# Optimization experiments

Hardware: AMD Instinct MI355X
Metric: run time of the kernel (lower is better)

## Reference

```python
import jax, jax.numpy as jnp
import numpy as np

N, D, E, OUT = 10000, 15, 320, 30
H_INOUT = 5  # n_heads for in/out attention layers


def mha(q, k, v, wqkv, bqkv, wo, bo, nheads):
    # q,k,v: [B, L, E]; torch.nn.MultiheadAttention math (unbatched per node)
    B, L, Ed = q.shape
    hd = Ed // nheads
    wq, wk, wv = jnp.split(wqkv, 3, axis=0)
    bq, bk, bv = jnp.split(bqkv, 3)
    q2 = (q @ wq.T + bq).reshape(B, L, nheads, hd)
    k2 = (k @ wk.T + bk).reshape(B, -1, nheads, hd)
    v2 = (v @ wv.T + bv).reshape(B, -1, nheads, hd)
    scores = jnp.einsum('blhd,bmhd->bhlm', q2, k2) * (hd ** -0.5)
    a = jax.nn.softmax(scores, axis=-1)
    o = jnp.einsum('bhlm,bmhd->blhd', a, v2).reshape(B, L, Ed)
    return o @ wo.T + bo


def attn_layer(seq, Wq, Wk, Wv, wqkv, bqkv, wo, bo, nheads):
    # AttentionLayer: custom Q/K/V projections then MultiheadAttention
    return mha(seq @ Wq, seq @ Wk, seq @ Wv, wqkv, bqkv, wo, bo, nheads)


def setup_inputs() -> dict:
    key = jax.random.key(0)
    ks = jax.random.split(key, 24)
    s = 0.05  # scale params small for numerically stable softmax
    inp = {
        'X': jax.random.normal(ks[0], (N, E), jnp.float32),
        'in_idx': jax.random.randint(ks[1], (N, D), 0, N),
        'out_idx': jax.random.randint(ks[2], (N, D), 0, N),
        'in_Wq': jax.random.uniform(ks[3], (E, E)) * s,
        'in_Wk': jax.random.uniform(ks[4], (E, E)) * s,
        'in_Wv': jax.random.uniform(ks[5], (E, E)) * s,
        'in_qkv_w': jax.random.normal(ks[6], (3 * E, E)) * s,
        'in_qkv_b': jax.random.normal(ks[7], (3 * E,)) * s,
        'in_o_w': jax.random.normal(ks[8], (E, E)) * s,
        'in_o_b': jax.random.normal(ks[9], (E,)) * s,
        'out_Wq': jax.random.uniform(ks[10], (E, E)) * s,
        'out_Wk': jax.random.uniform(ks[11], (E, E)) * s,
        'out_Wv': jax.random.uniform(ks[12], (E, E)) * s,
        'out_qkv_w': jax.random.normal(ks[13], (3 * E, E)) * s,
        'out_qkv_b': jax.random.normal(ks[14], (3 * E,)) * s,
        'out_o_w': jax.random.normal(ks[15], (E, E)) * s,
        'out_o_b': jax.random.normal(ks[16], (E,)) * s,
        'fin_qkv_w': jax.random.normal(ks[17], (3 * E, E)) * s,
        'fin_qkv_b': jax.random.normal(ks[18], (3 * E,)) * s,
        'fin_o_w': jax.random.normal(ks[19], (E, E)) * s,
        'fin_o_b': jax.random.normal(ks[20], (E,)) * s,
        'W': jax.random.uniform(ks[21], (E, OUT)) * s,
    }
    return inp


def reference(X, in_idx, out_idx, in_Wq, in_Wk, in_Wv, in_qkv_w, in_qkv_b,
              in_o_w, in_o_b, out_Wq, out_Wk, out_Wv, out_qkv_w, out_qkv_b,
              out_o_w, out_o_b, fin_qkv_w, fin_qkv_b, fin_o_w, fin_o_b, W):
    # per-node sequence: [self ; neighbors] -> [N, D+1, E]
    seq_in = jnp.concatenate([X[:, None, :], X[in_idx]], axis=1)
    seq_out = jnp.concatenate([X[:, None, :], X[out_idx]], axis=1)
    a_in = attn_layer(seq_in, in_Wq, in_Wk, in_Wv, in_qkv_w, in_qkv_b,
                      in_o_w, in_o_b, H_INOUT)
    a_out = attn_layer(seq_out, out_Wq, out_Wk, out_Wv, out_qkv_w, out_qkv_b,
                       out_o_w, out_o_b, H_INOUT)
    att = jnp.concatenate([a_in, a_out], axis=1)  # [N, 2(D+1), E]
    fin = mha(att, att, att, fin_qkv_w, fin_qkv_b, fin_o_w, fin_o_b, 1)
    # first token of final attention per node -> project -> ELU
    return jax.nn.elu(fin[:, 0, :] @ W)
```

## Files before the change

### kernel.cpp

```cpp
#include <hip/hip_runtime.h>
#include <hip/hip_bf16.h>

typedef __hip_bfloat16 bf16;
typedef __bf16 nbf;
typedef nbf bf16x8 __attribute__((ext_vector_type(8)));
typedef float f32x4 __attribute__((ext_vector_type(4)));

#define NNODE 10000
#define DDEG  15
#define EE    320
#define LL    16
#define NH    5
#define HD    64
#define OUTD  30
#define PCOLS 1920
#define KF    642
#define TSTB  648

__global__ void detect_dtype_kernel(const unsigned int* __restrict__ X, int* __restrict__ flag)
{
    __shared__ int cnt;
    if (threadIdx.x == 0) cnt = 0;
    __syncthreads();
    int local = 0;
    for (int i = threadIdx.x; i < 1024; i += 256) {
        unsigned int lo = X[i] & 0xFFFFu;
        int e = (int)((lo >> 7) & 0xFFu);
        if (e >= 100 && e <= 140) local++;
    }
    atomicAdd(&cnt, local);
    __syncthreads();
    if (threadIdx.x == 0) *flag = (cnt > 512) ? 1 : 0;
}

__global__ void convert_bf_kernel(const void* __restrict__ src, nbf* __restrict__ dst,
                                  int n, const int* __restrict__ flag)
{
    int i = blockIdx.x * 256 + threadIdx.x;
    if (i >= n) return;
    if (*flag) dst[i] = ((const nbf*)src)[i];
    else       dst[i] = (nbf)(((const float*)src)[i]);
}

#define NSEG 18
struct ConvTab {
    const void* src[NSEG];
    void*       dst[NSEG];
    int         n[NSEG];
    int         tobf[NSEG];
};

__global__ void convert_batch_kernel(ConvTab t, const int* __restrict__ flag)
{
    const int seg = blockIdx.y;
    const int i = blockIdx.x * 256 + threadIdx.x;
    if (i >= t.n[seg]) return;
    float v = (*flag) ? (float)(((const nbf*)t.src[seg])[i]) : ((const float*)t.src[seg])[i];
    if (t.tobf[seg]) ((nbf*)t.dst[seg])[i] = (nbf)v;
    else             ((float*)t.dst[seg])[i] = v;
}

__global__ __launch_bounds__(256) void transpose3_kernel(const void* s0, const void* s1,
        const void* s2, nbf* __restrict__ dstbase, const int* __restrict__ flag)
{
    const void* src = (blockIdx.z == 0) ? s0 : (blockIdx.z == 1) ? s1 : s2;
    nbf* dst = dstbase + (size_t)blockIdx.z * EE * EE;
    __shared__ nbf tile[32][33];
    const int bx = blockIdx.x * 32, by = blockIdx.y * 32;
    const int tx = threadIdx.x & 31, ty = threadIdx.x >> 5;
    const int f = *flag;
    #pragma unroll
    for (int i = 0; i < 4; ++i) {
        const int r = by + ty + i * 8;
        float v = f ? (float)(((const nbf*)src)[(long)r * EE + bx + tx])
                    : ((const float*)src)[(long)r * EE + bx + tx];
        tile[ty + i * 8][tx] = (nbf)v;
    }
    __syncthreads();
    #pragma unroll
    for (int i = 0; i < 4; ++i) {
        const int r = bx + ty + i * 8;
        dst[(long)r * EE + by + tx] = tile[tx][ty + i * 8];
    }
}

__device__ __forceinline__ void stor(float* p, float v) { *p = v; }
__device__ __forceinline__ void stor(bf16* p, float v) { *p = __float2bfloat16(v); }

template<bool AT, bool BT, typename OT>
__global__ __launch_bounds__(256) void gemm_k(const float* __restrict__ A, int lda,
                       const float* __restrict__ B, int ldb,
                       const float* __restrict__ bias,
                       OT* __restrict__ C, int ldc, int M, int Nn, int K)
{
    __shared__ float As[16][65];
    __shared__ float Bs[16][65];
    const int tid = threadIdx.x;
    const int tx = tid & 15, ty = tid >> 4;
    const int n0 = blockIdx.x * 64, m0 = blockIdx.y * 64;
    float acc[4][4] = {};
    for (int k0 = 0; k0 < K; k0 += 16) {
        if constexpr (AT) {
            for (int i = tid; i < 1024; i += 256) {
                int kk = i >> 6, r = i & 63;
                int gm = m0 + r, gk = k0 + kk;
                As[kk][r] = (gm < M && gk < K) ? A[(long)gk * lda + gm] : 0.f;
            }
        } else {
            for (int i = tid; i < 1024; i += 256) {
                int r = i >> 4, kk = i & 15;
                int gm = m0 + r, gk = k0 + kk;
                As[kk][r] = (gm < M && gk < K) ? A[(long)gm * lda + gk] : 0.f;
            }
        }
        if constexpr (BT) {
            for (int i = tid; i < 1024; i += 256) {
                int r = i >> 4, kk = i & 15;
                int gn = n0 + r, gk = k0 + kk;
                Bs[kk][r] = (gn < Nn && gk < K) ? B[(long)gn * ldb + gk] : 0.f;
            }
        } else {
            for (int i = tid; i < 1024; i += 256) {
                int kk = i >> 6, c = i & 63;
                int gk = k0 + kk, gn = n0 + c;
                Bs[kk][c] = (gk < K && gn < Nn) ? B[(long)gk * ldb + gn] : 0.f;
            }
        }
        __syncthreads();
        #pragma unroll
        for (int kk = 0; kk < 16; ++kk) {
            float ra[4], rb[4];
            #pragma unroll
            for (int a = 0; a < 4; ++a) ra[a] = As[kk][ty * 4 + a];
            #pragma unroll
            for (int b = 0; b < 4; ++b) rb[b] = Bs[kk][tx * 4 + b];
            #pragma unroll
            for (int a = 0; a < 4; ++a)
                #pragma unroll
                for (int b = 0; b < 4; ++b)
                    acc[a][b] += ra[a] * rb[b];
        }
        __syncthreads();
    }
    #pragma unroll
    for (int a = 0; a < 4; ++a) {
        int gm = m0 + ty * 4 + a;
        if (gm >= M) continue;
        #pragma unroll
        for (int b = 0; b < 4; ++b) {
            int gn = n0 + tx * 4 + b;
            if (gn >= Nn) continue;
            float v = acc[a][b] + (bias ? bias[gn] : 0.f);
            stor(&C[(long)gm * ldc + gn], v);
        }
    }
}

template<typename OT>
__global__ __launch_bounds__(256) void gemm_mfma(const nbf* __restrict__ A, int lda,
        const nbf* __restrict__ Bt, int ldb, const float* __restrict__ bias,
        OT* __restrict__ C, int ldc, int M, int Nn, int K)
{
    __shared__ __align__(16) nbf As[128][40];
    __shared__ __align__(16) nbf Bs[128][40];
    const int tid = threadIdx.x;
    const int lane = tid & 63, wave = tid >> 6;
    const int wr = (wave >> 1) * 64, wc = (wave & 1) * 64;
    const int m0 = blockIdx.y * 128, n0 = blockIdx.x * 128;
    const int lr = lane & 15, lq = lane >> 4;
    f32x4 acc[4][4];
    #pragma unroll
    for (int i = 0; i < 4; ++i)
        #pragma unroll
        for (int j = 0; j < 4; ++j) { acc[i][j][0]=0.f; acc[i][j][1]=0.f; acc[i][j][2]=0.f; acc[i][j][3]=0.f; }

    for (int k0 = 0; k0 < K; k0 += 32) {
        #pragma unroll
        for (int v = tid; v < 512; v += 256) {
            const int row = v >> 2, cv = (v & 3) << 3;
            const int gk = k0 + cv;
            {
                const int gm = m0 + row;
                bf16x8 val;
                if (gm < M && gk + 8 <= K) {
                    val = *(const bf16x8*)(A + (long)gm * lda + gk);
                } else {
                    union { bf16x8 v8; nbf e[8]; } u;
                    #pragma unroll
                    for (int j = 0; j < 8; ++j) {
                        float x = (gm < M && gk + j < K) ? (float)A[(long)gm * lda + gk + j] : 0.f;
                        u.e[j] = (nbf)x;
                    }
                    val = u.v8;
                }
                *(bf16x8*)&As[row][cv] = val;
            }
            {
                const int gn = n0 + row;
                bf16x8 val;
                if (gn < Nn && gk + 8 <= K) {
                    val = *(const bf16x8*)(Bt + (long)gn * ldb + gk);
                } else {
                    union { bf16x8 v8; nbf e[8]; } u;
                    #pragma unroll
                    for (int j = 0; j < 8; ++j) {
                        float x = (gn < Nn && gk + j < K) ? (float)Bt[(long)gn * ldb + gk + j] : 0.f;
                        u.e[j] = (nbf)x;
                    }
                    val = u.v8;
                }
                *(bf16x8*)&Bs[row][cv] = val;
            }
        }
        __syncthreads();
        bf16x8 af[4], bfv[4];
        #pragma unroll
        for (int i = 0; i < 4; ++i) af[i] = *(const bf16x8*)&As[wr + i * 16 + lr][lq * 8];
        #pragma unroll
        for (int j = 0; j < 4; ++j) bfv[j] = *(const bf16x8*)&Bs[wc + j * 16 + lr][lq * 8];
        #pragma unroll
        for (int i = 0; i < 4; ++i)
            #pragma unroll
            for (int j = 0; j < 4; ++j)
                acc[i][j] = __builtin_amdgcn_mfma_f32_16x16x32_bf16(af[i], bfv[j], acc[i][j], 0, 0, 0);
        __syncthreads();
    }
    #pragma unroll
    for (int i = 0; i < 4; ++i) {
        #pragma unroll
        for (int j = 0; j < 4; ++j) {
            const int gn = n0 + wc + j * 16 + lr;
            if (gn >= Nn) continue;
            const float bv = bias ? bias[gn] : 0.f;
            #pragma unroll
            for (int r = 0; r < 4; ++r) {
                const int gm = m0 + wr + i * 16 + lq * 4 + r;
                if (gm < M) stor(&C[(long)gm * ldc + gn], acc[i][j][r] + bv);
            }
        }
    }
}

#define NJOB 11
struct JobTab {
    const nbf* A[NJOB];
    const nbf* B[NJOB];
    nbf*       C[NJOB];
};

__global__ __launch_bounds__(256) void gemm_mfma_jobs(JobTab jt)
{
    const nbf* A  = jt.A[blockIdx.z];
    const nbf* Bt = jt.B[blockIdx.z];
    nbf* C        = jt.C[blockIdx.z];
    __shared__ __align__(16) nbf As[128][40];
    __shared__ __align__(16) nbf Bs[128][40];
    const int tid = threadIdx.x;
    const int lane = tid & 63, wave = tid >> 6;
    const int wr = (wave >> 1) * 64, wc = (wave & 1) * 64;
    const int m0 = blockIdx.y * 128, n0 = blockIdx.x * 128;
    const int lr = lane & 15, lq = lane >> 4;
    f32x4 acc[4][4];
    #pragma unroll
    for (int i = 0; i < 4; ++i)
        #pragma unroll
        for (int j = 0; j < 4; ++j) { acc[i][j][0]=0.f; acc[i][j][1]=0.f; acc[i][j][2]=0.f; acc[i][j][3]=0.f; }
    for (int k0 = 0; k0 < EE; k0 += 32) {
        #pragma unroll
        for (int v = tid; v < 512; v += 256) {
            const int row = v >> 2, cv = (v & 3) << 3;
            const int gk = k0 + cv;
            const int gm = m0 + row, gn = n0 + row;
            bf16x8 va = {}, vb = {};
            if (gm < EE) va = *(const bf16x8*)(A + (long)gm * EE + gk);
            if (gn < EE) vb = *(const bf16x8*)(Bt + (long)gn * EE + gk);
            *(bf16x8*)&As[row][cv] = va;
            *(bf16x8*)&Bs[row][cv] = vb;
        }
        __syncthreads();
        bf16x8 af[4], bfv[4];
        #pragma unroll
        for (int i = 0; i < 4; ++i) af[i] = *(const bf16x8*)&As[wr + i * 16 + lr][lq * 8];
        #pragma unroll
        for (int j = 0; j < 4; ++j) bfv[j] = *(const bf16x8*)&Bs[wc + j * 16 + lr][lq * 8];
        #pragma unroll
        for (int i = 0; i < 4; ++i)
            #pragma unroll
            for (int j = 0; j < 4; ++j)
                acc[i][j] = __builtin_amdgcn_mfma_f32_16x16x32_bf16(af[i], bfv[j], acc[i][j], 0, 0, 0);
        __syncthreads();
    }
    #pragma unroll
    for (int i = 0; i < 4; ++i)
        #pragma unroll
        for (int j = 0; j < 4; ++j) {
            const int gn = n0 + wc + j * 16 + lr;
            if (gn >= EE) continue;
            #pragma unroll
            for (int r = 0; r < 4; ++r) {
                const int gm = m0 + wr + i * 16 + lq * 4 + r;
                if (gm < EE) C[(long)gm * EE + gn] = (nbf)acc[i][j][r];
            }
        }
}

__global__ __launch_bounds__(320) void compose_bias_kernel(
        const float* __restrict__ in_o_b, const float* __restrict__ out_o_b,
        const float* __restrict__ fin_qkv_w, const float* __restrict__ fin_qkv_b,
        float* __restrict__ bqc_in, nbf* __restrict__ Kcat, nbf* __restrict__ VcatN)
{
    const int which = blockIdx.x;
    const int b = threadIdx.x;
    const float* ob = (which == 2 || which == 4) ? out_o_b : in_o_b;
    const int off = (which == 0) ? 0 : (which <= 2) ? 320 : 640;
    float acc = fin_qkv_b[off + b];
    const float* wr = fin_qkv_w + (long)(off + b) * EE;
    for (int e = 0; e < EE; ++e) acc += ob[e] * wr[e];
    if (which == 0)      bqc_in[b] = acc;
    else if (which == 1) Kcat[(long)640 * EE + b] = (nbf)acc;
    else if (which == 2) Kcat[(long)641 * EE + b] = (nbf)acc;
    else if (which == 3) VcatN[(long)640 * EE + b] = (nbf)acc;
    else                 VcatN[(long)641 * EE + b] = (nbf)acc;
}

__global__ void compose_bfin(const float* __restrict__ fin_o_b, const float* __restrict__ W,
                             float* __restrict__ bfin)
{
    int j = threadIdx.x;
    if (j >= OUTD) return;
    float acc = 0.f;
    for (int e = 0; e < EE; ++e) acc += fin_o_b[e] * W[e * OUTD + j];
    bfin[j] = acc;
}

__global__ void compose_bT(const float* __restrict__ bqc, const nbf* __restrict__ Kcat,
                           float* __restrict__ bT)
{
    int c = blockIdx.x * 256 + threadIdx.x;
    if (c >= KF) return;
    const nbf* kr = Kcat + (long)c * EE;
    float acc = 0.f;
    for (int b = 0; b < EE; ++b) acc += bqc[b] * (float)kr[b];
    bT[c] = acc;
}

__global__ void ut_prep_kernel(const float* __restrict__ WWT, nbf* __restrict__ Ut)
{
    int v = blockIdx.x * 256 + threadIdx.x;
    if (v >= 64 * EE) return;
    int n = v / EE, e = v % EE;
    float val = 0.f;
    if (n < OUTD) val = WWT[(long)n * KF + e];
    else if (n >= 32 && n < 32 + OUTD) val = WWT[(long)(n - 32) * KF + 320 + e];
    Ut[v] = (nbf)val;
}

__global__ __launch_bounds__(256) void row0_kernel(const nbf* __restrict__ P,
        const int* __restrict__ in_idx, nbf* __restrict__ Orow0)
{
    const int tid = threadIdx.x, lane = tid & 63, wave = tid >> 6;
    const int node = blockIdx.x * 4 + wave;
    __shared__ float a_sh[4][16];
    __shared__ int srcs_sh[4][16];
    const int m = lane & 15, q4 = lane >> 4;
    const int src = (m == 0) ? node : in_idx[node * DDEG + m - 1];
    if (q4 == 0) srcs_sh[wave][m] = src;
    const nbf* qrow = P + (long)node * PCOLS;
    const nbf* krow = P + (long)src * PCOLS + 320;
    #pragma unroll
    for (int h = 0; h < NH; ++h) {
        float s = 0.f;
        bf16x8 q1 = *(const bf16x8*)(qrow + h * 64 + q4 * 16);
        bf16x8 q2 = *(const bf16x8*)(qrow + h * 64 + q4 * 16 + 8);
        bf16x8 k1 = *(const bf16x8*)(krow + h * 64 + q4 * 16);
        bf16x8 k2 = *(const bf16x8*)(krow + h * 64 + q4 * 16 + 8);
        #pragma unroll
        for (int j = 0; j < 8; ++j)
            s += (float)q1[j] * (float)k1[j] + (float)q2[j] * (float)k2[j];
        s += __shfl_xor(s, 16);
        s += __shfl_xor(s, 32);
        s *= 0.125f;
        float mxv = s;
        #pragma unroll
        for (int msk = 8; msk >= 1; msk >>= 1) mxv = fmaxf(mxv, __shfl_xor(mxv, msk));
        float e = __expf(s - mxv);
        float es = e;
        #pragma unroll
        for (int msk = 8; msk >= 1; msk >>= 1) es += __shfl_xor(es, msk);
        if (q4 == 0) a_sh[wave][m] = e / es;
        float o = 0.f;
        #pragma unroll
        for (int mm = 0; mm < 16; ++mm)
            o += a_sh[wave][mm] * (float)P[(long)srcs_sh[wave][mm] * PCOLS + 640 + h * 64 + lane];
        Orow0[(long)node * EE + h * 64 + lane] = (nbf)o;
    }
}

__global__ __launch_bounds__(320) void attn_y_kernel(const nbf* __restrict__ P,
        const int* __restrict__ in_idx, const int* __restrict__ out_idx,
        const nbf* __restrict__ Tb, const nbf* __restrict__ Ut,
        float* __restrict__ Ygl, int node_base)
{
    const int bx = blockIdx.x;
    const int lnode = bx >> 1, d = bx & 1;
    const int node = node_base + lnode;
    const int tid = threadIdx.x;
    const int lane = tid & 63, wave = tid >> 6;
    __shared__ __align__(16) nbf v_s[16][328];
    __shared__ __align__(16) nbf p_s[NH][16][16];
    __shared__ float Yp[NH][16][32];
    const int* idx = d ? out_idx : in_idx;
    const long coloff = (long)d * 960;
    const int lr = lane & 15, lq = lane >> 4;
    #pragma unroll
    for (int v = tid; v < 640; v += 320) {
        const int row = v / 40, c8 = (v % 40) * 8;
        const int src = (row == 0) ? node : idx[node * DDEG + row - 1];
        *(bf16x8*)&v_s[row][c8] = *(const bf16x8*)(P + (long)src * PCOLS + coloff + 640 + c8);
    }
    const int msrc = (lr == 0) ? node : idx[node * DDEG + lr - 1];
    const nbf* prow = P + (long)msrc * PCOLS + coloff;
    f32x4 sc = {0.f, 0.f, 0.f, 0.f};
    #pragma unroll
    for (int c = 0; c < 2; ++c) {
        bf16x8 aq = *(const bf16x8*)(prow + wave * 64 + c * 32 + lq * 8);
        bf16x8 bk = *(const bf16x8*)(prow + 320 + wave * 64 + c * 32 + lq * 8);
        sc = __builtin_amdgcn_mfma_f32_16x16x32_bf16(aq, bk, sc, 0, 0, 0);
    }
    float pr[4], mx4[4], sm4[4];
    #pragma unroll
    for (int r = 0; r < 4; ++r) { pr[r] = sc[r] * 0.125f; mx4[r] = pr[r]; }
    #pragma unroll
    for (int msk = 8; msk >= 1; msk >>= 1)
        #pragma unroll
        for (int r = 0; r < 4; ++r) mx4[r] = fmaxf(mx4[r], __shfl_xor(mx4[r], msk));
    #pragma unroll
    for (int r = 0; r < 4; ++r) { pr[r] = __expf(pr[r] - mx4[r]); sm4[r] = pr[r]; }
    #pragma unroll
    for (int msk = 8; msk >= 1; msk >>= 1)
        #pragma unroll
        for (int r = 0; r < 4; ++r) sm4[r] += __shfl_xor(sm4[r], msk);
    #pragma unroll
    for (int r = 0; r < 4; ++r) p_s[wave][lq * 4 + r][lr] = (nbf)(pr[r] / sm4[r]);
    union { bf16x8 v8; nbf e[8]; } pf;
    #pragma unroll
    for (int j = 0; j < 8; ++j) pf.e[j] = (nbf)0.f;
    if (lq < 2) pf.v8 = *(const bf16x8*)&p_s[wave][lr][lq * 8];
    __syncthreads();
    #pragma unroll
    for (int t = 0; t < 4; ++t) {
        const int e0 = wave * 64 + t * 16;
        union { bf16x8 v8; nbf e[8]; } af;
        #pragma unroll
        for (int j = 0; j < 8; ++j) af.e[j] = (nbf)0.f;
        if (lq < 2) {
            #pragma unroll
            for (int j = 0; j < 8; ++j) af.e[j] = v_s[lq * 8 + j][e0 + lr];
        }
        f32x4 ov = {0.f, 0.f, 0.f, 0.f};
        ov = __builtin_amdgcn_mfma_f32_16x16x32_bf16(af.v8, pf.v8, ov, 0, 0, 0);
        union { unsigned long long u; nbf e[4]; } o4;
        #pragma unroll
        for (int r = 0; r < 4; ++r) o4.e[r] = (nbf)ov[r];
        *(unsigned long long*)&v_s[lr][e0 + lq * 4] = o4.u;
    }
    const nbf* Utd = Ut + (long)d * 32 * EE;
    const nbf* TbRow = Tb + (long)node * TSTB + (long)d * 320;
    f32x4 yacc[2];
    yacc[0][0]=0.f; yacc[0][1]=0.f; yacc[0][2]=0.f; yacc[0][3]=0.f;
    yacc[1][0]=0.f; yacc[1][1]=0.f; yacc[1][2]=0.f; yacc[1][3]=0.f;
    const int e0w = wave * 64;
    #pragma unroll
    for (int c = 0; c < 2; ++c) {
        const int kk = e0w + c * 32 + lq * 8;
        bf16x8 afy = *(const bf16x8*)&v_s[lr][kk];
        #pragma unroll
        for (int nt = 0; nt < 2; ++nt) {
            const int row = nt * 16 + lr;
            const nbf* bp = (row == 31) ? (TbRow + kk) : (Utd + (long)row * EE + kk);
            bf16x8 bfy = *(const bf16x8*)bp;
            yacc[nt] = __builtin_amdgcn_mfma_f32_16x16x32_bf16(afy, bfy, yacc[nt], 0, 0, 0);
        }
    }
    #pragma unroll
    for (int nt = 0; nt < 2; ++nt)
        #pragma unroll
        for (int r = 0; r < 4; ++r)
            Yp[wave][lq * 4 + r][nt * 16 + lr] = yacc[nt][r];
    __syncthreads();
    float* yout = Ygl + (long)(lnode * 2 + d) * 512;
    for (int v = tid; v < 512; v += 320) {
        float sme = 0.f;
        #pragma unroll
        for (int w = 0; w < NH; ++w) sme += Yp[w][v >> 5][v & 31];
        yout[v] = sme;
    }
}

__global__ __launch_bounds__(256) void combine_kernel(const float* __restrict__ Ygl,
        const nbf* __restrict__ Tb, const float* __restrict__ WWT,
        const float* __restrict__ bfin, void* __restrict__ out,
        long obase, int cnt, const int* __restrict__ flag)
{
    const int tid = threadIdx.x, lane = tid & 63, wave = tid >> 6;
    const int node = blockIdx.x * 4 + wave;
    const int nodec = (node < cnt) ? node : (cnt - 1);
    __shared__ float Yl[4][1024];
    __shared__ float sf[4][32];
    const float* ysrc = Ygl + (long)nodec * 1024;
    #pragma unroll
    for (int v = lane; v < 1024; v += 64) Yl[wave][v] = ysrc[v];
    if (lane < 32) {
        const int d = lane >> 4, m = lane & 15;
        sf[wave][lane] = (Yl[wave][d * 512 + m * 32 + 31]
                          + (float)Tb[(long)nodec * TSTB + 640 + d]) * 0.05590169943749474f;
    }
    float mx = -1e30f;
    #pragma unroll 4
    for (int m = 0; m < 32; ++m) mx = fmaxf(mx, sf[wave][m]);
    float esum = 0.f, a_in = 0.f, a_out = 0.f;
    #pragma unroll 4
    for (int m = 0; m < 32; ++m) {
        float e = __expf(sf[wave][m] - mx);
        esum += e;
        if (m < 16) a_in += e; else a_out += e;
    }
    const float inv = 1.f / esum;
    a_in *= inv; a_out *= inv;
    const int j = lane;
    if (j < OUTD && node < cnt) {
        float acc = 0.f;
        #pragma unroll 4
        for (int dm = 0; dm < 32; ++dm) {
            const int d = dm >> 4, m = dm & 15;
            float a = __expf(sf[wave][dm] - mx) * inv;
            acc += a * Yl[wave][d * 512 + m * 32 + j];
        }
        float r = acc + a_in * WWT[(long)j * KF + 640]
                + a_out * WWT[(long)j * KF + 641] + bfin[j];
        r = r > 0.f ? r : expm1f(r);
        if (*flag) ((bf16*)out)[obase + (long)node * OUTD + j] = __float2bfloat16(r);
        else       ((float*)out)[obase + (long)node * OUTD + j] = r;
    }
}

extern "C" void kernel_launch(void* const* d_in, const int* in_sizes, int n_in,
                              void* d_out, int out_size, void* d_ws, size_t ws_size,
                              hipStream_t stream)
{
    const int* in_idx  = (const int*)d_in[1];
    const int* out_idx = (const int*)d_in[2];

    char* p = (char*)d_ws;
    auto alloc = [&](size_t bytes) { char* r = p; p += (bytes + 255) & ~(size_t)255; return r; };
    const size_t EE2 = (size_t)EE * EE;
    int*   flag       = (int*)alloc(256);
    nbf*   X_bf       = (nbf*)alloc((size_t)NNODE * EE * 2);
    nbf*   qkvw6_bf   = (nbf*)alloc(6 * EE2 * 2);
    nbf*   Wg6_bf     = (nbf*)alloc(6 * EE2 * 2);
    nbf*   qkvw_fin_bf= (nbf*)alloc(3 * EE2 * 2);
    nbf*   owT        = (nbf*)alloc(3 * EE2 * 2);
    float* qkvw_fin_f = (float*)alloc(3 * EE2 * 4);
    float* qkvb_fin_f = (float*)alloc(3 * EE * 4);
    float* bcat       = (float*)alloc(PCOLS * 4);
    float* ob_in_f    = (float*)alloc(EE * 4);
    float* ob_out_f   = (float*)alloc(EE * 4);
    float* ob_fin_f   = (float*)alloc(EE * 4);
    float* W_f        = (float*)alloc((size_t)EE * OUTD * 4);
    float* ow_fin_f   = (float*)alloc(EE2 * 4);
    nbf*   AcatT  = (nbf*)alloc((size_t)PCOLS * EE * 2);
    nbf*   Qc_bf  = (nbf*)alloc(EE2 * 2);
    nbf*   Kcat   = (nbf*)alloc((size_t)KF * EE * 2);
    float* bqc_in = (float*)alloc(EE * 4);
    nbf*   M2T    = (nbf*)alloc((size_t)KF * EE * 2);
    float* bT     = (float*)alloc(KF * 4);
    nbf*   VcatN  = (nbf*)alloc((size_t)KF * EE * 2);
    nbf*   WfinT  = (nbf*)alloc((size_t)OUTD * EE * 2);
    float* WWT    = (float*)alloc((size_t)OUTD * KF * 4);
    float* bfin   = (float*)alloc(64 * 4);
    nbf*   Ut     = (nbf*)alloc((size_t)64 * EE * 2);
    nbf*   P      = (nbf*)alloc((size_t)NNODE * PCOLS * 2);
    nbf*   Orow0  = (nbf*)alloc((size_t)NNODE * EE * 2);
    nbf*   Tb     = (nbf*)alloc((size_t)NNODE * TSTB * 2);
    size_t fixed = (size_t)(p - (char*)d_ws);

    const size_t per_node = 1024 * 4;
    size_t avail = (ws_size > fixed + 65536) ? (ws_size - fixed - 65536) : 0;
    long chunk_l = (long)(avail / per_node);
    chunk_l = (chunk_l / 4) * 4;
    int chunk = (chunk_l > NNODE) ? NNODE : (chunk_l < 4 ? 4 : (int)chunk_l);
    float* Ygl = (float*)alloc((size_t)chunk * 1024 * 4);

    dim3 blk(256);
    detect_dtype_kernel<<<1, blk, 0, stream>>>((const unsigned int*)d_in[0], flag);
    convert_bf_kernel<<<(NNODE * EE + 255) / 256, blk, 0, stream>>>(d_in[0], X_bf, NNODE * EE, flag);
    ConvTab ct;
    int s = 0;
    auto seg = [&](const void* src, void* dst, int n, int tobf) {
        ct.src[s] = src; ct.dst[s] = dst; ct.n[s] = n; ct.tobf[s] = tobf; ++s;
    };
    seg(d_in[6],  qkvw6_bf,           (int)(3 * EE2), 1);
    seg(d_in[13], qkvw6_bf + 3 * EE2, (int)(3 * EE2), 1);
    seg(d_in[3],  Wg6_bf + 0 * EE2, (int)EE2, 1);
    seg(d_in[4],  Wg6_bf + 1 * EE2, (int)EE2, 1);
    seg(d_in[5],  Wg6_bf + 2 * EE2, (int)EE2, 1);
    seg(d_in[10], Wg6_bf + 3 * EE2, (int)EE2, 1);
    seg(d_in[11], Wg6_bf + 4 * EE2, (int)EE2, 1);
    seg(d_in[12], Wg6_bf + 5 * EE2, (int)EE2, 1);
    seg(d_in[17], qkvw_fin_bf, (int)(3 * EE2), 1);
    seg(d_in[17], qkvw_fin_f,  (int)(3 * EE2), 0);
    seg(d_in[18], qkvb_fin_f, 3 * EE, 0);
    seg(d_in[7],  bcat,       3 * EE, 0);
    seg(d_in[14], bcat + 960, 3 * EE, 0);
    seg(d_in[9],  ob_in_f,  EE, 0);
    seg(d_in[16], ob_out_f, EE, 0);
    seg(d_in[20], ob_fin_f, EE, 0);
    seg(d_in[21], W_f, EE * OUTD, 0);
    seg(d_in[19], ow_fin_f, (int)EE2, 0);
    convert_batch_kernel<<<dim3((3 * (int)EE2 + 255) / 256, NSEG), blk, 0, stream>>>(ct, flag);
    transpose3_kernel<<<dim3(10, 10, 3), blk, 0, stream>>>(d_in[8], d_in[15], d_in[19], owT, flag);

    JobTab jt;
    for (int g = 0; g < 6; ++g) {
        jt.A[g] = qkvw6_bf + (size_t)g * EE2;
        jt.B[g] = Wg6_bf + (size_t)g * EE2;
        jt.C[g] = AcatT + (size_t)g * EE2;
    }
    jt.A[6] = owT;             jt.B[6] = qkvw_fin_bf;                      jt.C[6] = Qc_bf;
    jt.A[7] = owT;             jt.B[7] = qkvw_fin_bf + (size_t)320 * EE;   jt.C[7] = Kcat;
    jt.A[8] = owT + EE2;       jt.B[8] = qkvw_fin_bf + (size_t)320 * EE;   jt.C[8] = Kcat + (size_t)320 * EE;
    jt.A[9] = owT;             jt.B[9] = qkvw_fin_bf + (size_t)640 * EE;   jt.C[9] = VcatN;
    jt.A[10]= owT + EE2;       jt.B[10]= qkvw_fin_bf + (size_t)640 * EE;   jt.C[10]= VcatN + (size_t)320 * EE;
    gemm_mfma_jobs<<<dim3(3, 3, NJOB), blk, 0, stream>>>(jt);
    compose_bias_kernel<<<5, 320, 0, stream>>>(ob_in_f, ob_out_f, qkvw_fin_f, qkvb_fin_f,
                                               bqc_in, Kcat, VcatN);
    gemm_mfma<bf16><<<dim3(3, 6), blk, 0, stream>>>(
        Kcat, EE, Qc_bf, EE, nullptr, (bf16*)M2T, EE, KF, EE, EE);
    compose_bT<<<3, blk, 0, stream>>>(bqc_in, Kcat, bT);
    gemm_k<true, false, bf16><<<dim3(5, 1), blk, 0, stream>>>(
        W_f, OUTD, ow_fin_f, EE, nullptr, (bf16*)WfinT, EE, OUTD, EE, EE);
    gemm_mfma<float><<<dim3(6, 1), blk, 0, stream>>>(
        WfinT, EE, VcatN, EE, nullptr, WWT, KF, OUTD, KF, EE);
    compose_bfin<<<1, 64, 0, stream>>>(ob_fin_f, W_f, bfin);
    ut_prep_kernel<<<(64 * EE + 255) / 256, blk, 0, stream>>>(WWT, Ut);

    gemm_mfma<bf16><<<dim3(PCOLS / 128, (NNODE + 127) / 128), blk, 0, stream>>>(
        X_bf, EE, AcatT, EE, bcat, (bf16*)P, PCOLS, NNODE, PCOLS, EE);

    row0_kernel<<<NNODE / 4, blk, 0, stream>>>(P, in_idx, Orow0);

    gemm_mfma<bf16><<<dim3((KF + 127) / 128, (NNODE + 127) / 128), blk, 0, stream>>>(
        Orow0, EE, M2T, EE, bT, (bf16*)Tb, TSTB, NNODE, KF, EE);

    for (int base = 0; base < NNODE; base += chunk) {
        int cnt = (NNODE - base < chunk) ? (NNODE - base) : chunk;
        attn_y_kernel<<<2 * cnt, dim3(320), 0, stream>>>(
            P, in_idx, out_idx, Tb, Ut, Ygl, base);
        combine_kernel<<<(cnt + 3) / 4, blk, 0, stream>>>(
            Ygl, Tb + (size_t)base * TSTB, WWT, bfin, d_out, (long)base * OUTD, cnt, flag);
    }
}
```

Measured before the change: 497.1 us.

## Merge preprocessing and weight-composition kernels into fewer launches, add fast GEMM tile path

Detect-dtype, X conversion, batched conversion and transposes are folded into one prep kernel. The small bias and weight-composition kernels are folded into an extra z-slice of the job GEMM plus a new finalize kernel. This cuts the number of tiny serial launches. The MFMA GEMM gets an unguarded load path for full tiles, and attn_y prefetches its Ut/Tb B-fragments into registers before the main work. The risks are more register pressure in attn_y and serial scalar loops in the merged tiny-work blocks.

```diff
diff --git a/kernel.cpp b/kernel.cpp
--- a/kernel.cpp
+++ b/kernel.cpp
@@ -9,152 +9,84 @@
 #define NNODE 10000
 #define DDEG  15
 #define EE    320
-#define LL    16
 #define NH    5
-#define HD    64
 #define OUTD  30
 #define PCOLS 1920
 #define KF    642
 #define TSTB  648
 
-__global__ void detect_dtype_kernel(const unsigned int* __restrict__ X, int* __restrict__ flag)
-{
-    __shared__ int cnt;
-    if (threadIdx.x == 0) cnt = 0;
+#define NSEG 18
+struct PrepTab {
+    const void* seg_src[NSEG];
+    void*       seg_dst[NSEG];
+    int         seg_n[NSEG];
+    int         seg_tobf[NSEG];
+    int         seg_blocks[NSEG];
+    const void* xsrc; nbf* xdst; int xblocks;
+    const void* tsrc0; const void* tsrc1; const void* tsrc2; nbf* tdst;
+    int* flag;
+};
+
+__global__ __launch_bounds__(256) void prep_kernel(PrepTab t)
+{
+    __shared__ int cnt_s;
+    __shared__ __align__(16) nbf tile[32][33];
+    if (threadIdx.x == 0) cnt_s = 0;
     __syncthreads();
-    int local = 0;
-    for (int i = threadIdx.x; i < 1024; i += 256) {
-        unsigned int lo = X[i] & 0xFFFFu;
-        int e = (int)((lo >> 7) & 0xFFu);
-        if (e >= 100 && e <= 140) local++;
-    }
-    atomicAdd(&cnt, local);
+    {
+        const unsigned int* Xw = (const unsigned int*)t.xsrc;
+        int local = 0;
+        for (int i = threadIdx.x; i < 1024; i += 256) {
+            unsigned int lo = Xw[i] & 0xFFFFu;
+            int e = (int)((lo >> 7) & 0xFFu);
+            if (e >= 100 && e <= 140) local++;
+        }
+        atomicAdd(&cnt_s, local);
+    }
     __syncthreads();
-    if (threadIdx.x == 0) *flag = (cnt > 512) ? 1 : 0;
-}
-
-__global__ void convert_bf_kernel(const void* __restrict__ src, nbf* __restrict__ dst,
-                                  int n, const int* __restrict__ flag)
-{
-    int i = blockIdx.x * 256 + threadIdx.x;
-    if (i >= n) return;
-    if (*flag) dst[i] = ((const nbf*)src)[i];
-    else       dst[i] = (nbf)(((const float*)src)[i]);
-}
-
-#define NSEG 18
-struct ConvTab {
-    const void* src[NSEG];
-    void*       dst[NSEG];
-    int         n[NSEG];
-    int         tobf[NSEG];
-};
-
-__global__ void convert_batch_kernel(ConvTab t, const int* __restrict__ flag)
-{
-    const int seg = blockIdx.y;
-    const int i = blockIdx.x * 256 + threadIdx.x;
-    if (i >= t.n[seg]) return;
-    float v = (*flag) ? (float)(((const nbf*)t.src[seg])[i]) : ((const float*)t.src[seg])[i];
-    if (t.tobf[seg]) ((nbf*)t.dst[seg])[i] = (nbf)v;
-    else             ((float*)t.dst[seg])[i] = v;
-}
-
-__global__ __launch_bounds__(256) void transpose3_kernel(const void* s0, const void* s1,
-        const void* s2, nbf* __restrict__ dstbase, const int* __restrict__ flag)
-{
-    const void* src = (blockIdx.z == 0) ? s0 : (blockIdx.z == 1) ? s1 : s2;
-    nbf* dst = dstbase + (size_t)blockIdx.z * EE * EE;
-    __shared__ nbf tile[32][33];
-    const int bx = blockIdx.x * 32, by = blockIdx.y * 32;
-    const int tx = threadIdx.x & 31, ty = threadIdx.x >> 5;
-    const int f = *flag;
-    #pragma unroll
-    for (int i = 0; i < 4; ++i) {
-        const int r = by + ty + i * 8;
-        float v = f ? (float)(((const nbf*)src)[(long)r * EE + bx + tx])
-                    : ((const float*)src)[(long)r * EE + bx + tx];
-        tile[ty + i * 8][tx] = (nbf)v;
-    }
-    __syncthreads();
-    #pragma unroll
-    for (int i = 0; i < 4; ++i) {
-        const int r = bx + ty + i * 8;
-        dst[(long)r * EE + by + tx] = tile[tx][ty + i * 8];
-    }
+    const int f = cnt_s > 512;
+    int b = blockIdx.x;
+    if (b == 0 && threadIdx.x == 0) *t.flag = f;
+    if (b < t.xblocks) {
+        int i = b * 256 + threadIdx.x;
+        if (i < NNODE * EE)
+            t.xdst[i] = f ? ((const nbf*)t.xsrc)[i] : (nbf)(((const float*)t.xsrc)[i]);
+        return;
+    }
+    b -= t.xblocks;
+    if (b < 300) {
+        const int z = b / 100, rem = b % 100;
+        const int by = (rem / 10) * 32, bx = (rem % 10) * 32;
+        const void* src = (z == 0) ? t.tsrc0 : (z == 1) ? t.tsrc1 : t.tsrc2;
+        nbf* dst = t.tdst + (size_t)z * EE * EE;
+        const int tx = threadIdx.x & 31, ty = threadIdx.x >> 5;
+        #pragma unroll
+        for (int i = 0; i < 4; ++i) {
+            const int r = by + ty + i * 8;
+            float v = f ? (float)(((const nbf*)src)[(long)r * EE + bx + tx])
+                        : ((const float*)src)[(long)r * EE + bx + tx];
+            tile[ty + i * 8][tx] = (nbf)v;
+        }
+        __syncthreads();
+        #pragma unroll
+        for (int i = 0; i < 4; ++i) {
+            const int r = bx + ty + i * 8;
+            dst[(long)r * EE + by + tx] = tile[tx][ty + i * 8];
+        }
+        return;
+    }
+    b -= 300;
+    int s = 0;
+    while (s < NSEG - 1 && b >= t.seg_blocks[s]) { b -= t.seg_blocks[s]; ++s; }
+    int i = b * 256 + threadIdx.x;
+    if (i >= t.seg_n[s]) return;
+    float v = f ? (float)(((const nbf*)t.seg_src[s])[i]) : ((const float*)t.seg_src[s])[i];
+    if (t.seg_tobf[s]) ((nbf*)t.seg_dst[s])[i] = (nbf)v;
+    else               ((float*)t.seg_dst[s])[i] = v;
 }
 
 __device__ __forceinline__ void stor(float* p, float v) { *p = v; }
 __device__ __forceinline__ void stor(bf16* p, float v) { *p = __float2bfloat16(v); }
-
-template<bool AT, bool BT, typename OT>
-__global__ __launch_bounds__(256) void gemm_k(const float* __restrict__ A, int lda,
-                       const float* __restrict__ B, int ldb,
-                       const float* __restrict__ bias,
-                       OT* __restrict__ C, int ldc, int M, int Nn, int K)
-{
-    __shared__ float As[16][65];
-    __shared__ float Bs[16][65];
-    const int tid = threadIdx.x;
-    const int tx = tid & 15, ty = tid >> 4;
-    const int n0 = blockIdx.x * 64, m0 = blockIdx.y * 64;
-    float acc[4][4] = {};
-    for (int k0 = 0; k0 < K; k0 += 16) {
-        if constexpr (AT) {
-            for (int i = tid; i < 1024; i += 256) {
-                int kk = i >> 6, r = i & 63;
-                int gm = m0 + r, gk = k0 + kk;
-                As[kk][r] = (gm < M && gk < K) ? A[(long)gk * lda + gm] : 0.f;
-            }
-        } else {
-            for (int i = tid; i < 1024; i += 256) {
-                int r = i >> 4, kk = i & 15;
-                int gm = m0 + r, gk = k0 + kk;
-                As[kk][r] = (gm < M && gk < K) ? A[(long)gm * lda + gk] : 0.f;
-            }
-        }
-        if constexpr (BT) {
-            for (int i = tid; i < 1024; i += 256) {
-                int r = i >> 4, kk = i & 15;
-                int gn = n0 + r, gk = k0 + kk;
-                Bs[kk][r] = (gn < Nn && gk < K) ? B[(long)gn * ldb + gk] : 0.f;
-            }
-        } else {
-            for (int i = tid; i < 1024; i += 256) {
-                int kk = i >> 6, c = i & 63;
-                int gk = k0 + kk, gn = n0 + c;
-                Bs[kk][c] = (gk < K && gn < Nn) ? B[(long)gk * ldb + gn] : 0.f;
-            }
-        }
-        __syncthreads();
-        #pragma unroll
-        for (int kk = 0; kk < 16; ++kk) {
-            float ra[4], rb[4];
-            #pragma unroll
-            for (int a = 0; a < 4; ++a) ra[a] = As[kk][ty * 4 + a];
-            #pragma unroll
-            for (int b = 0; b < 4; ++b) rb[b] = Bs[kk][tx * 4 + b];
-            #pragma unroll
-            for (int a = 0; a < 4; ++a)
-                #pragma unroll
-                for (int b = 0; b < 4; ++b)
-                    acc[a][b] += ra[a] * rb[b];
-        }
-        __syncthreads();
-    }
-    #pragma unroll
-    for (int a = 0; a < 4; ++a) {
-        int gm = m0 + ty * 4 + a;
-        if (gm >= M) continue;
-        #pragma unroll
-        for (int b = 0; b < 4; ++b) {
-            int gn = n0 + tx * 4 + b;
-            if (gn >= Nn) continue;
-            float v = acc[a][b] + (bias ? bias[gn] : 0.f);
-            stor(&C[(long)gm * ldc + gn], v);
-        }
-    }
-}
 
 template<typename OT>
 __global__ __launch_bounds__(256) void gemm_mfma(const nbf* __restrict__ A, int lda,
@@ -168,6 +100,7 @@
     const int wr = (wave >> 1) * 64, wc = (wave & 1) * 64;
     const int m0 = blockIdx.y * 128, n0 = blockIdx.x * 128;
     const int lr = lane & 15, lq = lane >> 4;
+    const bool full = (m0 + 128 <= M) && (n0 + 128 <= Nn);
     f32x4 acc[4][4];
     #pragma unroll
     for (int i = 0; i < 4; ++i)
@@ -175,41 +108,51 @@
         for (int j = 0; j < 4; ++j) { acc[i][j][0]=0.f; acc[i][j][1]=0.f; acc[i][j][2]=0.f; acc[i][j][3]=0.f; }
 
     for (int k0 = 0; k0 < K; k0 += 32) {
-        #pragma unroll
-        for (int v = tid; v < 512; v += 256) {
-            const int row = v >> 2, cv = (v & 3) << 3;
-            const int gk = k0 + cv;
-            {
-                const int gm = m0 + row;
-                bf16x8 val;
-                if (gm < M && gk + 8 <= K) {
-                    val = *(const bf16x8*)(A + (long)gm * lda + gk);
-                } else {
-                    union { bf16x8 v8; nbf e[8]; } u;
-                    #pragma unroll
-                    for (int j = 0; j < 8; ++j) {
-                        float x = (gm < M && gk + j < K) ? (float)A[(long)gm * lda + gk + j] : 0.f;
-                        u.e[j] = (nbf)x;
+        if (full) {
+            #pragma unroll
+            for (int v = tid; v < 512; v += 256) {
+                const int row = v >> 2, cv = (v & 3) << 3;
+                const int gk = k0 + cv;
+                *(bf16x8*)&As[row][cv] = *(const bf16x8*)(A + (long)(m0 + row) * lda + gk);
+                *(bf16x8*)&Bs[row][cv] = *(const bf16x8*)(Bt + (long)(n0 + row) * ldb + gk);
+            }
+        } else {
+            #pragma unroll
+            for (int v = tid; v < 512; v += 256) {
+                const int row = v >> 2, cv = (v & 3) << 3;
+                const int gk = k0 + cv;
+                {
+                    const int gm = m0 + row;
+                    bf16x8 val;
+                    if (gm < M && gk + 8 <= K) {
+                        val = *(const bf16x8*)(A + (long)gm * lda + gk);
+                    } else {
+                        union { bf16x8 v8; nbf e[8]; } u;
+                        #pragma unroll
+                        for (int j = 0; j < 8; ++j) {
+                            float x = (gm < M && gk + j < K) ? (float)A[(long)gm * lda + gk + j] : 0.f;
+                            u.e[j] = (nbf)x;
+                        }
+                        val = u.v8;
                     }
-                    val = u.v8;
+                    *(bf16x8*)&As[row][cv] = val;
                 }
-                *(bf16x8*)&As[row][cv] = val;
-            }
-            {
-                const int gn = n0 + row;
-                bf16x8 val;
-                if (gn < Nn && gk + 8 <= K) {
-                    val = *(const bf16x8*)(Bt + (long)gn * ldb + gk);
-                } else {
-                    union { bf16x8 v8; nbf e[8]; } u;
-                    #pragma unroll
-                    for (int j = 0; j < 8; ++j) {
-                        float x = (gn < Nn && gk + j < K) ? (float)Bt[(long)gn * ldb + gk + j] : 0.f;
-                        u.e[j] = (nbf)x;
+                {
+                    const int gn = n0 + row;
+                    bf16x8 val;
+                    if (gn < Nn && gk + 8 <= K) {
+                        val = *(const bf16x8*)(Bt + (long)gn * ldb + gk);
+                    } else {
+                        union { bf16x8 v8; nbf e[8]; } u;
+                        #pragma unroll
+                        for (int j = 0; j < 8; ++j) {
+                            float x = (gn < Nn && gk + j < K) ? (float)Bt[(long)gn * ldb + gk + j] : 0.f;
+                            u.e[j] = (nbf)x;
+                        }
+                        val = u.v8;
                     }
-                    val = u.v8;
+                    *(bf16x8*)&Bs[row][cv] = val;
                 }
-                *(bf16x8*)&Bs[row][cv] = val;
             }
         }
         __syncthreads();
@@ -248,14 +191,52 @@
     nbf*       C[NJOB];
 };
 
-__global__ __launch_bounds__(256) void gemm_mfma_jobs(JobTab jt)
-{
+__global__ __launch_bounds__(256) void gemm_mfma_jobs(JobTab jt,
+        const float* __restrict__ qkvw_fin_f, const float* __restrict__ qkvb_fin_f,
+        const float* __restrict__ ob_in_f, const float* __restrict__ ob_out_f,
+        const float* __restrict__ ob_fin_f, const float* __restrict__ W_f,
+        const float* __restrict__ ow_fin_f,
+        float* __restrict__ bqc_in, float* __restrict__ bfin,
+        float* __restrict__ WfinT_f, nbf* __restrict__ Kcat, nbf* __restrict__ VcatN)
+{
+    const int tid = threadIdx.x;
+    if (blockIdx.z == NJOB) {
+        const int t9 = blockIdx.y * 3 + blockIdx.x;
+        if (t9 < 5) {
+            const float* ob = (t9 == 2 || t9 == 4) ? ob_out_f : ob_in_f;
+            const int off = (t9 == 0) ? 0 : (t9 <= 2) ? 320 : 640;
+            for (int bb = tid; bb < EE; bb += 256) {
+                float acc = qkvb_fin_f[off + bb];
+                const float* wr = qkvw_fin_f + (long)(off + bb) * EE;
+                for (int e = 0; e < EE; ++e) acc += ob[e] * wr[e];
+                if (t9 == 0)      bqc_in[bb] = acc;
+                else if (t9 == 1) Kcat[(long)640 * EE + bb] = (nbf)acc;
+                else if (t9 == 2) Kcat[(long)641 * EE + bb] = (nbf)acc;
+                else if (t9 == 3) VcatN[(long)640 * EE + bb] = (nbf)acc;
+                else              VcatN[(long)641 * EE + bb] = (nbf)acc;
+            }
+        } else if (t9 == 5) {
+            for (int j = tid; j < OUTD; j += 256) {
+                float acc = 0.f;
+                for (int e = 0; e < EE; ++e) acc += ob_fin_f[e] * W_f[e * OUTD + j];
+                bfin[j] = acc;
+            }
+        } else if (t9 == 6) {
+            for (int v = tid; v < OUTD * EE; v += 256) {
+                const int j = v / EE, e = v % EE;
+                float acc = 0.f;
+                for (int a = 0; a < EE; ++a)
+                    acc += W_f[a * OUTD + j] * ow_fin_f[(long)a * EE + e];
+                WfinT_f[v] = acc;
+            }
+        }
+        return;
+    }
     const nbf* A  = jt.A[blockIdx.z];
     const nbf* Bt = jt.B[blockIdx.z];
     nbf* C        = jt.C[blockIdx.z];
     __shared__ __align__(16) nbf As[128][40];
     __shared__ __align__(16) nbf Bs[128][40];
-    const int tid = threadIdx.x;
     const int lane = tid & 63, wave = tid >> 6;
     const int wr = (wave >> 1) * 64, wc = (wave & 1) * 64;
     const int m0 = blockIdx.y * 128, n0 = blockIdx.x * 128;
@@ -304,55 +285,102 @@
         }
 }
 
-__global__ __launch_bounds__(320) void compose_bias_kernel(
-        const float* __restrict__ in_o_b, const float* __restrict__ out_o_b,
-        const float* __restrict__ fin_qkv_w, const float* __restrict__ fin_qkv_b,
-        float* __restrict__ bqc_in, nbf* __restrict__ Kcat, nbf* __restrict__ VcatN)
-{
-    const int which = blockIdx.x;
-    const int b = threadIdx.x;
-    const float* ob = (which == 2 || which == 4) ? out_o_b : in_o_b;
-    const int off = (which == 0) ? 0 : (which <= 2) ? 320 : 640;
-    float acc = fin_qkv_b[off + b];
-    const float* wr = fin_qkv_w + (long)(off + b) * EE;
-    for (int e = 0; e < EE; ++e) acc += ob[e] * wr[e];
-    if (which == 0)      bqc_in[b] = acc;
-    else if (which == 1) Kcat[(long)640 * EE + b] = (nbf)acc;
-    else if (which == 2) Kcat[(long)641 * EE + b] = (nbf)acc;
-    else if (which == 3) VcatN[(long)640 * EE + b] = (nbf)acc;
-    else                 VcatN[(long)641 * EE + b] = (nbf)acc;
-}
-
-__global__ void compose_bfin(const float* __restrict__ fin_o_b, const float* __restrict__ W,
-                             float* __restrict__ bfin)
-{
-    int j = threadIdx.x;
-    if (j >= OUTD) return;
-    float acc = 0.f;
-    for (int e = 0; e < EE; ++e) acc += fin_o_b[e] * W[e * OUTD + j];
-    bfin[j] = acc;
-}
-
-__global__ void compose_bT(const float* __restrict__ bqc, const nbf* __restrict__ Kcat,
-                           float* __restrict__ bT)
-{
-    int c = blockIdx.x * 256 + threadIdx.x;
-    if (c >= KF) return;
-    const nbf* kr = Kcat + (long)c * EE;
-    float acc = 0.f;
-    for (int b = 0; b < EE; ++b) acc += bqc[b] * (float)kr[b];
-    bT[c] = acc;
-}
-
-__global__ void ut_prep_kernel(const float* __restrict__ WWT, nbf* __restrict__ Ut)
-{
-    int v = blockIdx.x * 256 + threadIdx.x;
-    if (v >= 64 * EE) return;
-    int n = v / EE, e = v % EE;
-    float val = 0.f;
-    if (n < OUTD) val = WWT[(long)n * KF + e];
-    else if (n >= 32 && n < 32 + OUTD) val = WWT[(long)(n - 32) * KF + 320 + e];
-    Ut[v] = (nbf)val;
+__global__ __launch_bounds__(256) void finalize_kernel(
+        const nbf* __restrict__ Kcat, const nbf* __restrict__ Qc,
+        const float* __restrict__ bqc, const nbf* __restrict__ VcatN,
+        const float* __restrict__ WfinT_f,
+        nbf* __restrict__ M2T, float* __restrict__ bT,
+        nbf* __restrict__ Ut, float* __restrict__ WWTa)
+{
+    __shared__ __align__(16) char smem[40960];
+    const int b = blockIdx.x;
+    const int tid = threadIdx.x;
+    if (b < 18) {
+        nbf (*As)[40] = (nbf(*)[40])smem;
+        nbf (*Bs)[40] = (nbf(*)[40])(smem + 10240);
+        const int lane = tid & 63, wave = tid >> 6;
+        const int wr = (wave >> 1) * 64, wc = (wave & 1) * 64;
+        const int m0 = (b / 3) * 128, n0 = (b % 3) * 128;
+        const int lr = lane & 15, lq = lane >> 4;
+        f32x4 acc[4][4];
+        #pragma unroll
+        for (int i = 0; i < 4; ++i)
+            #pragma unroll
+            for (int j = 0; j < 4; ++j) { acc[i][j][0]=0.f; acc[i][j][1]=0.f; acc[i][j][2]=0.f; acc[i][j][3]=0.f; }
+        for (int k0 = 0; k0 < EE; k0 += 32) {
+            #pragma unroll
+            for (int v = tid; v < 512; v += 256) {
+                const int row = v >> 2, cv = (v & 3) << 3;
+                const int gk = k0 + cv;
+                const int gm = m0 + row, gn = n0 + row;
+                bf16x8 va = {}, vb = {};
+                if (gm < KF) va = *(const bf16x8*)(Kcat + (long)gm * EE + gk);
+                if (gn < EE) vb = *(const bf16x8*)(Qc + (long)gn * EE + gk);
+                *(bf16x8*)&As[row][cv] = va;
+                *(bf16x8*)&Bs[row][cv] = vb;
+            }
+            __syncthreads();
+            bf16x8 af[4], bfv[4];
+            #pragma unroll
+            for (int i = 0; i < 4; ++i) af[i] = *(const bf16x8*)&As[wr + i * 16 + lr][lq * 8];
+            #pragma unroll
+            for (int j = 0; j < 4; ++j) bfv[j] = *(const bf16x8*)&Bs[wc + j * 16 + lr][lq * 8];
+            #pragma unroll
+            for (int i = 0; i < 4; ++i)
+                #pragma unroll
+                for (int j = 0; j < 4; ++j)
+                    acc[i][j] = __builtin_amdgcn_mfma_f32_16x16x32_bf16(af[i], bfv[j], acc[i][j], 0, 0, 0);
+            __syncthreads();
+        }
+        #pragma unroll
+        for (int i = 0; i < 4; ++i)
+            #pragma unroll
+            for (int j = 0; j < 4; ++j) {
+                const int gn = n0 + wc + j * 16 + lr;
+                if (gn >= EE) continue;
+                #pragma unroll
+                for (int r = 0; r < 4; ++r) {
+                    const int gm = m0 + wr + i * 16 + lq * 4 + r;
+                    if (gm < KF) M2T[(long)gm * EE + gn] = (nbf)acc[i][j][r];
+                }
+            }
+        return;
+    }
+    if (b < 21) {
+        const int c = (b - 18) * 256 + tid;
+        if (c < KF) {
+            const nbf* kr = Kcat + (long)c * EE;
+            float acc = 0.f;
+            for (int e = 0; e < EE; ++e) acc += bqc[e] * (float)kr[e];
+            bT[c] = acc;
+        }
+        return;
+    }
+    const int d = b - 21;
+    float (*Wf)[EE] = (float(*)[EE])smem;
+    for (int v = tid; v < OUTD * EE; v += 256) Wf[v / EE][v % EE] = WfinT_f[v];
+    __syncthreads();
+    if (tid < OUTD) {
+        const nbf* vr = VcatN + (long)(640 + d) * EE;
+        float acc = 0.f;
+        for (int e = 0; e < EE; ++e) acc += Wf[tid][e] * (float)vr[e];
+        WWTa[tid * 2 + d] = acc;
+    }
+    for (int v = tid; v < 2 * EE; v += 256)
+        Ut[(long)(d * 32 + 30 + v / EE) * EE + (v % EE)] = (nbf)0.f;
+    for (int e = tid; e < EE; e += 256) {
+        const nbf* vrow = VcatN + (long)(d * 320 + e) * EE;
+        float acc[OUTD];
+        #pragma unroll
+        for (int j = 0; j < OUTD; ++j) acc[j] = 0.f;
+        for (int a = 0; a < EE; ++a) {
+            const float v = (float)vrow[a];
+            #pragma unroll
+            for (int j = 0; j < OUTD; ++j) acc[j] += Wf[j][a] * v;
+        }
+        for (int j = 0; j < OUTD; ++j)
+            Ut[(long)(d * 32 + j) * EE + e] = (nbf)acc[j];
+    }
 }
 
 __global__ __launch_bounds__(256) void row0_kernel(const nbf* __restrict__ P,
@@ -412,6 +440,18 @@
     const int* idx = d ? out_idx : in_idx;
     const long coloff = (long)d * 960;
     const int lr = lane & 15, lq = lane >> 4;
+    const nbf* Utd = Ut + (long)d * 32 * EE;
+    const nbf* TbRow = Tb + (long)node * TSTB + (long)d * 320;
+    bf16x8 yb[2][2];
+    #pragma unroll
+    for (int c = 0; c < 2; ++c)
+        #pragma unroll
+        for (int nt = 0; nt < 2; ++nt) {
+            const int kk = wave * 64 + c * 32 + lq * 8;
+            const int row = nt * 16 + lr;
+            yb[c][nt] = *(const bf16x8*)((row == 31) ? (TbRow + kk)
+                                                     : (Utd + (long)row * EE + kk));
+        }
     #pragma unroll
     for (int v = tid; v < 640; v += 320) {
         const int row = v / 40, c8 = (v % 40) * 8;
@@ -464,8 +504,6 @@
         for (int r = 0; r < 4; ++r) o4.e[r] = (nbf)ov[r];
         *(unsigned long long*)&v_s[lr][e0 + lq * 4] = o4.u;
     }
-    const nbf* Utd = Ut + (long)d * 32 * EE;
-    const nbf* TbRow = Tb + (long)node * TSTB + (long)d * 320;
     f32x4 yacc[2];
     yacc[0][0]=0.f; yacc[0][1]=0.f; yacc[0][2]=0.f; yacc[0][3]=0.f;
     yacc[1][0]=0.f; yacc[1][1]=0.f; yacc[1][2]=0.f; yacc[1][3]=0.f;
@@ -475,12 +513,8 @@
         const int kk = e0w + c * 32 + lq * 8;
         bf16x8 afy = *(const bf16x8*)&v_s[lr][kk];
         #pragma unroll
-        for (int nt = 0; nt < 2; ++nt) {
-            const int row = nt * 16 + lr;
-            const nbf* bp = (row == 31) ? (TbRow + kk) : (Utd + (long)row * EE + kk);
-            bf16x8 bfy = *(const bf16x8*)bp;
-            yacc[nt] = __builtin_amdgcn_mfma_f32_16x16x32_bf16(afy, bfy, yacc[nt], 0, 0, 0);
-        }
+        for (int nt = 0; nt < 2; ++nt)
+            yacc[nt] = __builtin_amdgcn_mfma_f32_16x16x32_bf16(afy, yb[c][nt], yacc[nt], 0, 0, 0);
     }
     #pragma unroll
     for (int nt = 0; nt < 2; ++nt)
@@ -498,7 +532,7 @@
 }
 
 __global__ __launch_bounds__(256) void combine_kernel(const float* __restrict__ Ygl,
-        const nbf* __restrict__ Tb, const float* __restrict__ WWT,
+        const nbf* __restrict__ Tb, const float* __restrict__ WWTa,
         const float* __restrict__ bfin, void* __restrict__ out,
         long obase, int cnt, const int* __restrict__ flag)
 {
@@ -536,8 +570,7 @@
             float a = __expf(sf[wave][dm] - mx) * inv;
             acc += a * Yl[wave][d * 512 + m * 32 + j];
         }
-        float r = acc + a_in * WWT[(long)j * KF + 640]
-                + a_out * WWT[(long)j * KF + 641] + bfin[j];
+        float r = acc + a_in * WWTa[j * 2] + a_out * WWTa[j * 2 + 1] + bfin[j];
         r = r > 0.f ? r : expm1f(r);
         if (*flag) ((bf16*)out)[obase + (long)node * OUTD + j] = __float2bfloat16(r);
         else       ((float*)out)[obase + (long)node * OUTD + j] = r;
@@ -575,8 +608,8 @@
     nbf*   M2T    = (nbf*)alloc((size_t)KF * EE * 2);
     float* bT     = (float*)alloc(KF * 4);
     nbf*   VcatN  = (nbf*)alloc((size_t)KF * EE * 2);
-    nbf*   WfinT  = (nbf*)alloc((size_t)OUTD * EE * 2);
-    float* WWT    = (float*)alloc((size_t)OUTD * KF * 4);
+    float* WfinT_f= (float*)alloc((size_t)OUTD * EE * 4);
+    float* WWTa   = (float*)alloc(64 * 4);
     float* bfin   = (float*)alloc(64 * 4);
     nbf*   Ut     = (nbf*)alloc((size_t)64 * EE * 2);
     nbf*   P      = (nbf*)alloc((size_t)NNODE * PCOLS * 2);
@@ -592,12 +625,14 @@
     float* Ygl = (float*)alloc((size_t)chunk * 1024 * 4);
 
     dim3 blk(256);
-    detect_dtype_kernel<<<1, blk, 0, stream>>>((const unsigned int*)d_in[0], flag);
-    convert_bf_kernel<<<(NNODE * EE + 255) / 256, blk, 0, stream>>>(d_in[0], X_bf, NNODE * EE, flag);
-    ConvTab ct;
+    PrepTab pt;
+    pt.xsrc = d_in[0]; pt.xdst = X_bf; pt.xblocks = (NNODE * EE + 255) / 256;
+    pt.tsrc0 = d_in[8]; pt.tsrc1 = d_in[15]; pt.tsrc2 = d_in[19]; pt.tdst = owT;
+    pt.flag = flag;
     int s = 0;
     auto seg = [&](const void* src, void* dst, int n, int tobf) {
-        ct.src[s] = src; ct.dst[s] = dst; ct.n[s] = n; ct.tobf[s] = tobf; ++s;
+        pt.seg_src[s] = src; pt.seg_dst[s] = dst; pt.seg_n[s] = n;
+        pt.seg_tobf[s] = tobf; pt.seg_blocks[s] = (n + 255) / 256; ++s;
     };
     seg(d_in[6],  qkvw6_bf,           (int)(3 * EE2), 1);
     seg(d_in[13], qkvw6_bf + 3 * EE2, (int)(3 * EE2), 1);
@@ -617,8 +652,9 @@
     seg(d_in[20], ob_fin_f, EE, 0);
     seg(d_in[21], W_f, EE * OUTD, 0);
     seg(d_in[19], ow_fin_f, (int)EE2, 0);
-    convert_batch_kernel<<<dim3((3 * (int)EE2 + 255) / 256, NSEG), blk, 0, stream>>>(ct, flag);
-    transpose3_kernel<<<dim3(10, 10, 3), blk, 0, stream>>>(d_in[8], d_in[15], d_in[19], owT, flag);
+    int total_blocks = pt.xblocks + 300;
+    for (int i = 0; i < NSEG; ++i) total_blocks += pt.seg_blocks[i];
+    prep_kernel<<<total_blocks, blk, 0, stream>>>(pt);
 
     JobTab jt;
     for (int g = 0; g < 6; ++g) {
@@ -626,26 +662,20 @@
         jt.B[g] = Wg6_bf + (size_t)g * EE2;
         jt.C[g] = AcatT + (size_t)g * EE2;
     }
-    jt.A[6] = owT;             jt.B[6] = qkvw_fin_bf;                      jt.C[6] = Qc_bf;
-    jt.A[7] = owT;             jt.B[7] = qkvw_fin_bf + (size_t)320 * EE;   jt.C[7] = Kcat;
-    jt.A[8] = owT + EE2;       jt.B[8] = qkvw_fin_bf + (size_t)320 * EE;   jt.C[8] = Kcat + (size_t)320 * EE;
-    jt.A[9] = owT;             jt.B[9] = qkvw_fin_bf + (size_t)640 * EE;   jt.C[9] = VcatN;
-    jt.A[10]= owT + EE2;       jt.B[10]= qkvw_fin_bf + (size_t)640 * EE;   jt.C[10]= VcatN + (size_t)320 * EE;
-    gemm_mfma_jobs<<<dim3(3, 3, NJOB), blk, 0, stream>>>(jt);
-    compose_bias_kernel<<<5, 320, 0, stream>>>(ob_in_f, ob_out_f, qkvw_fin_f, qkvb_fin_f,
-                                               bqc_in, Kcat, VcatN);
-    gemm_mfma<bf16><<<dim3(3, 6), blk, 0, stream>>>(
-        Kcat, EE, Qc_bf, EE, nullptr, (bf16*)M2T, EE, KF, EE, EE);
-    compose_bT<<<3, blk, 0, stream>>>(bqc_in, Kcat, bT);
-    gemm_k<true, false, bf16><<<dim3(5, 1), blk, 0, stream>>>(
-        W_f, OUTD, ow_fin_f, EE, nullptr, (bf16*)WfinT, EE, OUTD, EE, EE);
-    gemm_mfma<float><<<dim3(6, 1), blk, 0, stream>>>(
-        WfinT, EE, VcatN, EE, nullptr, WWT, KF, OUTD, KF, EE);
-    compose_bfin<<<1, 64, 0, stream>>>(ob_fin_f, W_f, bfin);
-    ut_prep_kernel<<<(64 * EE + 255) / 256, blk, 0, stream>>>(WWT, Ut);
+    jt.A[6] = owT;        jt.B[6] = qkvw_fin_bf;                      jt.C[6] = Qc_bf;
+    jt.A[7] = owT;        jt.B[7] = qkvw_fin_bf + (size_t)320 * EE;   jt.C[7] = Kcat;
+    jt.A[8] = owT + EE2;  jt.B[8] = qkvw_fin_bf + (size_t)320 * EE;   jt.C[8] = Kcat + (size_t)320 * EE;
+    jt.A[9] = owT;        jt.B[9] = qkvw_fin_bf + (size_t)640 * EE;   jt.C[9] = VcatN;
+    jt.A[10]= owT + EE2;  jt.B[10]= qkvw_fin_bf + (size_t)640 * EE;   jt.C[10]= VcatN + (size_t)320 * EE;
+    gemm_mfma_jobs<<<dim3(3, 3, NJOB + 1), blk, 0, stream>>>(jt,
+        qkvw_fin_f, qkvb_fin_f, ob_in_f, ob_out_f, ob_fin_f, W_f, ow_fin_f,
+        bqc_in, bfin, WfinT_f, Kcat, VcatN);
 
     gemm_mfma<bf16><<<dim3(PCOLS / 128, (NNODE + 127) / 128), blk, 0, stream>>>(
         X_bf, EE, AcatT, EE, bcat, (bf16*)P, PCOLS, NNODE, PCOLS, EE);
+
+    finalize_kernel<<<23, blk, 0, stream>>>(Kcat, Qc_bf, bqc_in, VcatN, WfinT_f,
+                                            M2T, bT, Ut, WWTa);
 
     row0_kernel<<<NNODE / 4, blk, 0, stream>>>(P, in_idx, Orow0);
 
@@ -657,6 +687,6 @@
         attn_y_kernel<<<2 * cnt, dim3(320), 0, stream>>>(
             P, in_idx, out_idx, Tb, Ut, Ygl, base);
         combine_kernel<<<(cnt + 3) / 4, blk, 0, stream>>>(
-            Ygl, Tb + (size_t)base * TSTB, WWT, bfin, d_out, (long)base * OUTD, cnt, flag);
-    }
-}
+            Ygl, Tb + (size_t)base * TSTB, WWTa, bfin, d_out, (long)base * OUTD, cnt, flag);
+    }
+}
```

Result: slower. 742.6 us (+49.4%).
